# Kernel optimization log

Hardware: AMD Instinct MI355X
Metric: run time of the kernel (lower is better)

The kernel has to match this reference:

```python
import jax, jax.numpy as jnp
import numpy as np

TAU = 1.0
BETA = 0.1
MIN_NORM = 1.0
B = 4194304


def setup_inputs() -> dict:
    key = jax.random.key(0)
    # positions spread over the four-well landscape (minima near (0.5+-1, 0.5+-1))
    batch = jax.random.normal(key, (B, 2), dtype=jnp.float32) * 1.5
    return {"batch": batch}


def reference(batch):
    batch = batch.reshape(-1, 2)
    u = batch[..., 0] - 0.5
    v = batch[..., 1] - 0.5

    # potential V4 = (u^2-1)^2 + (v^2-1)^2 + beta*u*v
    energy = (u * u - 1.0) ** 2 + (v * v - 1.0) ** 2 + BETA * u * v

    # analytic gradient, forces = -grad
    gx = 4.0 * u * (u * u - 1.0) + BETA * v
    gy = 4.0 * v * (v * v - 1.0) + BETA * u
    forces = -jnp.stack((gx, gy), axis=-1)  # (B, 2)

    # analytic Hessian (B, 2, 2)
    hxx = 12.0 * (u * u) - 4.0
    hyy = 12.0 * (v * v) - 4.0
    hxy = jnp.full_like(hxx, BETA)
    hessian = jnp.stack(
        (jnp.stack((hxx, hxy), axis=-1), jnp.stack((hxy, hyy), axis=-1)), axis=-2
    )

    # eigh: ascending eigenvalues, matching torch.linalg.eigh convention
    eigenvals, eigenvecs = jnp.linalg.eigh(hessian)
    smallest_eigvec = eigenvecs[..., :, 0]  # (B, 2)

    # GAD direction: reflect forces along smallest-eigenvalue eigenvector
    gad = -forces + 2.0 * jnp.sum(forces * smallest_eigvec, axis=-1, keepdims=True) * smallest_eigvec

    # norm_gad_outside_ts branch: normalize gad outside saddle region if small
    eigval_product = eigenvals[..., 0] * eigenvals[..., 1]
    gad_mag = jnp.linalg.norm(gad, axis=-1, keepdims=True)  # (B, 1)
    mask = (eigval_product > 0) & (gad_mag[..., 0] < MIN_NORM)
    gad = jnp.where(mask[..., None], gad / jnp.maximum(gad_mag, 1e-30), gad)

    energy_grad = gad / TAU
    return energy, forces, energy_grad, hessian, eigenvals[..., 0], eigenvals[..., 1]
```

## Files before the change

kernel.cpp:

```cpp
#include <hip/hip_runtime.h>


typedef float f2v __attribute__((ext_vector_type(2)));
typedef float f4v __attribute__((ext_vector_type(4)));

__global__ __launch_bounds__(256, 8) void fw_energy_gad_kernel(
    const f2v* __restrict__ in, float* __restrict__ out, int n) {
    int i = blockIdx.x * blockDim.x + threadIdx.x;
    if (i >= n) return;

    const float BETA = 0.1f;

    f2v p = in[i];
    float u = p.x - 0.5f;
    float v = p.y - 0.5f;
    float uu = u * u;
    float vv = v * v;
    float a = uu - 1.0f;
    float b = vv - 1.0f;

    float energy = a * a + b * b + BETA * u * v;

    float gx = 4.0f * u * a + BETA * v;
    float gy = 4.0f * v * b + BETA * u;
    float fx = -gx;
    float fy = -gy;

    float hxx = 12.0f * uu - 4.0f;
    float hyy = 12.0f * vv - 4.0f;

    float d = 0.5f * (hxx - hyy);
    float m = 0.5f * (hxx + hyy);
    float r = __builtin_amdgcn_sqrtf(d * d + BETA * BETA);
    float l0 = m - r;
    float l1 = m + r;

    bool pos = (d >= 0.0f);
    float wx = pos ? BETA : (d - r);
    float wy = pos ? -(d + r) : BETA;
    float n2 = wx * wx + wy * wy;

    float fd = fx * wx + fy * wy;
    float s = (2.0f * fd) * __builtin_amdgcn_rcpf(n2);
    float gadx = -fx + s * wx;
    float gady = -fy + s * wy;

    float prod = l0 * l1;
    float g2 = gadx * gadx + gady * gady;
    if (prod > 0.0f && g2 < 1.0f) {
        float inv = __builtin_amdgcn_rsqf(fmaxf(g2, 1e-60f));
        gadx *= inv;
        gady *= inv;
    }

    size_t N = (size_t)n;
    float* e_out  = out;
    f2v*   f_out  = (f2v*)(out + N);
    f2v*   g_out  = (f2v*)(out + 3 * N);
    f4v*   h_out  = (f4v*)(out + 5 * N);
    float* l0_out = out + 9 * N;
    float* l1_out = out + 10 * N;

    __builtin_nontemporal_store(energy, e_out + i);
    f2v fo; fo.x = fx; fo.y = fy;
    __builtin_nontemporal_store(fo, f_out + i);
    f2v go; go.x = gadx; go.y = gady;
    __builtin_nontemporal_store(go, g_out + i);
    f4v ho; ho.x = hxx; ho.y = BETA; ho.z = BETA; ho.w = hyy;
    __builtin_nontemporal_store(ho, h_out + i);
    __builtin_nontemporal_store(l0, l0_out + i);
    __builtin_nontemporal_store(l1, l1_out + i);
}

extern "C" void kernel_launch(void* const* d_in, const int* in_sizes, int n_in,
                              void* d_out, int out_size, void* d_ws, size_t ws_size,
                              hipStream_t stream) {
    const f2v* in = (const f2v*)d_in[0];
    float* out = (float*)d_out;
    int n = in_sizes[0] / 2;

    int block = 256;
    int grid = (n + block - 1) / block;
    fw_energy_gad_kernel<<<grid, block, 0, stream>>>(in, out, n);
}
```

Before: 201.9 us.

## Restructure kernel to output-flat mapping with one 16-byte store per thread

```diff
diff --git a/kernel.cpp b/kernel.cpp
--- a/kernel.cpp
+++ b/kernel.cpp
@@ -4,82 +4,164 @@
 typedef float f2v __attribute__((ext_vector_type(2)));
 typedef float f4v __attribute__((ext_vector_type(4)));
 
-__global__ __launch_bounds__(256, 8) void fw_energy_gad_kernel(
+namespace {
+
+struct P { float u, v, uu, vv, a, b; };
+
+__device__ __forceinline__ P pre(float px, float py) {
+    P o;
+    o.u = px - 0.5f;
+    o.v = py - 0.5f;
+    o.uu = o.u * o.u;
+    o.vv = o.v * o.v;
+    o.a = o.uu - 1.0f;
+    o.b = o.vv - 1.0f;
+    return o;
+}
+
+__device__ __forceinline__ float energyf(const P& p) {
+    return p.a * p.a + p.b * p.b + 0.1f * p.u * p.v;
+}
+
+__device__ __forceinline__ f2v forcef(const P& p) {
+    f2v f;
+    f.x = -(4.0f * p.u * p.a + 0.1f * p.v);
+    f.y = -(4.0f * p.v * p.b + 0.1f * p.u);
+    return f;
+}
+
+__device__ __forceinline__ f2v eigf(const P& p) {
+    float hxx = 12.0f * p.uu - 4.0f;
+    float hyy = 12.0f * p.vv - 4.0f;
+    float d = 0.5f * (hxx - hyy);
+    float m = 0.5f * (hxx + hyy);
+    float r = __builtin_amdgcn_sqrtf(d * d + 0.01f);
+    f2v e; e.x = m - r; e.y = m + r;
+    return e;
+}
+
+__device__ __forceinline__ f2v gradf(const P& p) {
+    float hxx = 12.0f * p.uu - 4.0f;
+    float hyy = 12.0f * p.vv - 4.0f;
+    float d = 0.5f * (hxx - hyy);
+    float m = 0.5f * (hxx + hyy);
+    float r = __builtin_amdgcn_sqrtf(d * d + 0.01f);
+    float l0 = m - r, l1 = m + r;
+    f2v f = forcef(p);
+    bool pos = (d >= 0.0f);
+    float wx = pos ? 0.1f : (d - r);
+    float wy = pos ? -(d + r) : 0.1f;
+    float n2 = wx * wx + wy * wy;
+    float fd = f.x * wx + f.y * wy;
+    float s = (2.0f * fd) * __builtin_amdgcn_rcpf(n2);
+    float gx = -f.x + s * wx;
+    float gy = -f.y + s * wy;
+    float g2 = gx * gx + gy * gy;
+    if (l0 * l1 > 0.0f && g2 < 1.0f) {
+        float inv = __builtin_amdgcn_rsqf(fmaxf(g2, 1e-60f));
+        gx *= inv;
+        gy *= inv;
+    }
+    f2v g; g.x = gx; g.y = gy;
+    return g;
+}
+
+}
+
+__global__ __launch_bounds__(256) void fw_flat_kernel(
+    const float* __restrict__ in, float* __restrict__ out, int n) {
+    const float BETA = 0.1f;
+    size_t n4 = (size_t)(n >> 2);
+    size_t q = (size_t)blockIdx.x * blockDim.x + threadIdx.x;
+    if (q >= 11 * n4) return;
+
+    const f2v* in2 = (const f2v*)in;
+    const f4v* in4 = (const f4v*)in;
+    f4v res;
+
+    if (q < n4) {
+        size_t t = q;
+        f4v A = in4[2 * t], B = in4[2 * t + 1];
+        res.x = energyf(pre(A.x, A.y));
+        res.y = energyf(pre(A.z, A.w));
+        res.z = energyf(pre(B.x, B.y));
+        res.w = energyf(pre(B.z, B.w));
+    } else if (q < 3 * n4) {
+        size_t t = q - n4;
+        f4v A = in4[t];
+        f2v f0 = forcef(pre(A.x, A.y));
+        f2v f1 = forcef(pre(A.z, A.w));
+        res.x = f0.x; res.y = f0.y; res.z = f1.x; res.w = f1.y;
+    } else if (q < 5 * n4) {
+        size_t t = q - 3 * n4;
+        f4v A = in4[t];
+        f2v g0 = gradf(pre(A.x, A.y));
+        f2v g1 = gradf(pre(A.z, A.w));
+        res.x = g0.x; res.y = g0.y; res.z = g1.x; res.w = g1.y;
+    } else if (q < 9 * n4) {
+        size_t t = q - 5 * n4;
+        f2v p = in2[t];
+        P pp = pre(p.x, p.y);
+        res.x = 12.0f * pp.uu - 4.0f;
+        res.y = BETA;
+        res.z = BETA;
+        res.w = 12.0f * pp.vv - 4.0f;
+    } else if (q < 10 * n4) {
+        size_t t = q - 9 * n4;
+        f4v A = in4[2 * t], B = in4[2 * t + 1];
+        res.x = eigf(pre(A.x, A.y)).x;
+        res.y = eigf(pre(A.z, A.w)).x;
+        res.z = eigf(pre(B.x, B.y)).x;
+        res.w = eigf(pre(B.z, B.w)).x;
+    } else {
+        size_t t = q - 10 * n4;
+        f4v A = in4[2 * t], B = in4[2 * t + 1];
+        res.x = eigf(pre(A.x, A.y)).y;
+        res.y = eigf(pre(A.z, A.w)).y;
+        res.z = eigf(pre(B.x, B.y)).y;
+        res.w = eigf(pre(B.z, B.w)).y;
+    }
+
+    ((f4v*)out)[q] = res;
+}
+
+__global__ __launch_bounds__(256) void fw_energy_gad_scalar(
     const f2v* __restrict__ in, float* __restrict__ out, int n) {
     int i = blockIdx.x * blockDim.x + threadIdx.x;
     if (i >= n) return;
-
     const float BETA = 0.1f;
-
-    f2v p = in[i];
-    float u = p.x - 0.5f;
-    float v = p.y - 0.5f;
-    float uu = u * u;
-    float vv = v * v;
-    float a = uu - 1.0f;
-    float b = vv - 1.0f;
-
-    float energy = a * a + b * b + BETA * u * v;
-
-    float gx = 4.0f * u * a + BETA * v;
-    float gy = 4.0f * v * b + BETA * u;
-    float fx = -gx;
-    float fy = -gy;
-
-    float hxx = 12.0f * uu - 4.0f;
-    float hyy = 12.0f * vv - 4.0f;
-
-    float d = 0.5f * (hxx - hyy);
-    float m = 0.5f * (hxx + hyy);
-    float r = __builtin_amdgcn_sqrtf(d * d + BETA * BETA);
-    float l0 = m - r;
-    float l1 = m + r;
-
-    bool pos = (d >= 0.0f);
-    float wx = pos ? BETA : (d - r);
-    float wy = pos ? -(d + r) : BETA;
-    float n2 = wx * wx + wy * wy;
-
-    float fd = fx * wx + fy * wy;
-    float s = (2.0f * fd) * __builtin_amdgcn_rcpf(n2);
-    float gadx = -fx + s * wx;
-    float gady = -fy + s * wy;
-
-    float prod = l0 * l1;
-    float g2 = gadx * gadx + gady * gady;
-    if (prod > 0.0f && g2 < 1.0f) {
-        float inv = __builtin_amdgcn_rsqf(fmaxf(g2, 1e-60f));
-        gadx *= inv;
-        gady *= inv;
-    }
-
+    f2v pt = in[i];
+    P p = pre(pt.x, pt.y);
+    float energy = energyf(p);
+    f2v f = forcef(p);
+    f2v e = eigf(p);
+    f2v g = gradf(p);
     size_t N = (size_t)n;
-    float* e_out  = out;
-    f2v*   f_out  = (f2v*)(out + N);
-    f2v*   g_out  = (f2v*)(out + 3 * N);
-    f4v*   h_out  = (f4v*)(out + 5 * N);
-    float* l0_out = out + 9 * N;
-    float* l1_out = out + 10 * N;
-
-    __builtin_nontemporal_store(energy, e_out + i);
-    f2v fo; fo.x = fx; fo.y = fy;
-    __builtin_nontemporal_store(fo, f_out + i);
-    f2v go; go.x = gadx; go.y = gady;
-    __builtin_nontemporal_store(go, g_out + i);
-    f4v ho; ho.x = hxx; ho.y = BETA; ho.z = BETA; ho.w = hyy;
-    __builtin_nontemporal_store(ho, h_out + i);
-    __builtin_nontemporal_store(l0, l0_out + i);
-    __builtin_nontemporal_store(l1, l1_out + i);
+    out[i] = energy;
+    ((f2v*)(out + N))[i] = f;
+    ((f2v*)(out + 3 * N))[i] = g;
+    f4v ho; ho.x = 12.0f * p.uu - 4.0f; ho.y = BETA; ho.z = BETA;
+    ho.w = 12.0f * p.vv - 4.0f;
+    ((f4v*)(out + 5 * N))[i] = ho;
+    out[9 * N + i] = e.x;
+    out[10 * N + i] = e.y;
 }
 
 extern "C" void kernel_launch(void* const* d_in, const int* in_sizes, int n_in,
                               void* d_out, int out_size, void* d_ws, size_t ws_size,
                               hipStream_t stream) {
-    const f2v* in = (const f2v*)d_in[0];
+    const float* in = (const float*)d_in[0];
     float* out = (float*)d_out;
     int n = in_sizes[0] / 2;
 
-    int block = 256;
-    int grid = (n + block - 1) / block;
-    fw_energy_gad_kernel<<<grid, block, 0, stream>>>(in, out, n);
+    if ((n & 3) == 0) {
+        size_t total = 11 * (size_t)(n >> 2);
+        int block = 256;
+        int grid = (int)((total + block - 1) / block);
+        fw_flat_kernel<<<grid, block, 0, stream>>>(in, out, n);
+    } else {
+        int block = 256;
+        int grid = (n + block - 1) / block;
+        fw_energy_gad_scalar<<<grid, block, 0, stream>>>((const f2v*)in, out, n);
+    }
 }
```

New measurement: 214.5 us. 6.3% more time.
